# Kernel optimization log

Hardware: AMD Instinct MI355X
Metric: run time of the kernel (lower is better)

## Reference

```python
import jax, jax.numpy as jnp
import numpy as np

LAM = 0.5
LAG = 1
ALPHA = 0.5
EPS = 1e-8


def setup_inputs() -> dict:
    key = jax.random.key(0)
    k1, k2, k3, k4 = jax.random.split(key, 4)
    B, T, F, H = 64, 4096, 64, 256
    return {
        "input": jax.random.normal(k1, (B, T, 1), dtype=jnp.float32),
        "target": jax.random.normal(k2, (B, T, 1), dtype=jnp.float32),
        "sequence": jax.random.normal(k3, (B, T, F), dtype=jnp.float32),
        "forget_gates": jax.random.uniform(k4, (B, T, H), dtype=jnp.float32),
    }


def reference(input, target, sequence, forget_gates):
    B, T, F = sequence.shape
    x = jnp.moveaxis(sequence, 1, 0)          # [T, B, F] time-major
    x_t = x[LAG:]                              # [T-LAG, B, F]
    x_lag = x[:-LAG]                           # [T-LAG, B, F]

    m0 = jnp.zeros((B, F), dtype=sequence.dtype)
    v0 = jnp.full((B, F), EPS, dtype=sequence.dtype)
    c0 = jnp.zeros((B, F), dtype=sequence.dtype)

    def step(carry, inp):
        m, v, c = carry
        xt, xl = inp
        m = LAM * m + (1.0 - LAM) * xt
        v = LAM * v + (1.0 - LAM) * (xt - m) ** 2
        c = LAM * c + (1.0 - LAM) * (xt - m) * (xl - m)
        ac = c / jnp.sqrt(v * v + EPS)         # matches torch: sqrt(var*var + eps)
        return (m, v, c), ac

    _, acs = jax.lax.scan(step, (m0, v0, c0), (x_t, x_lag))  # [T-LAG, B, F]
    pad = jnp.zeros((LAG, B, F), dtype=sequence.dtype)       # initial_padding zeros
    ac_full = jnp.concatenate([pad, acs], axis=0)            # [T, B, F]

    irrelevance = 1.0 - jnp.abs(ac_full)                     # [T, B, F]
    irrelevance = jnp.mean(irrelevance, axis=2, keepdims=True)  # [T, B, 1]
    irrelevance = jnp.moveaxis(irrelevance, 0, 1)            # [B, T, 1]

    penalty = jnp.mean(irrelevance * forget_gates)
    mse = jnp.mean((input - target) ** 2)
    return mse + ALPHA * penalty
```

## Files before the change

### kernel.cpp

```cpp
#include <hip/hip_runtime.h>

constexpr int B = 64;
constexpr int T = 4096;
constexpr int F = 64;
constexpr int H = 256;
constexpr float EPSC = 1e-8f;
constexpr float ALPHAC = 0.5f;

constexpr int C = 128;
constexpr int W = 48;
constexpr int CHUNKS = T / C;
constexpr int NTASK = B * CHUNKS;
constexpr int SCAN_BLOCKS = NTASK / 4;
constexpr int TILE = 32;

constexpr int DOT_BLOCKS = 2048;

#define WS_IRR 0
#define WS_PEN (B * T)
#define WS_MSE (B * T + DOT_BLOCKS)

__global__ __launch_bounds__(256) void k_scan(
    const float* __restrict__ seq,
    const float* __restrict__ inp,
    const float* __restrict__ tgt,
    float* __restrict__ ws) {
  __shared__ float lt[4][TILE][65];
  const int lane = threadIdx.x & 63;
  const int wv = threadIdx.x >> 6;
  const int task = blockIdx.x * 4 + wv;
  const int b = task / CHUNKS;
  const int ci = task % CHUNKS;
  const int t0 = ci * C;

  const float* sp = seq + (size_t)b * T * F + lane;

  float m = 0.f, v = 0.f, c = 0.f;
  float xl = 0.f;

  if (ci == 0) {
    v = EPSC;
  } else {
    const int ts = t0 - W;
    xl = sp[(ts - 1) * F];
    float xw[4];
#pragma unroll
    for (int j = 0; j < 4; ++j) xw[j] = sp[(ts + j) * F];
#pragma unroll
    for (int i = 0; i < W; ++i) {
      const float xt = xw[i & 3];
      if (i + 4 < W) xw[i & 3] = sp[(ts + i + 4) * F];
      m = 0.5f * (m + xt);
      const float d = xt - m;
      v = 0.5f * fmaf(d, d, v);
      c = 0.5f * fmaf(d, xl - m, c);
      xl = xt;
    }
  }

  float xb[8];
#pragma unroll
  for (int j = 0; j < 8; ++j) xb[j] = sp[(t0 + j) * F];

  const int tr = lane & 31;
  const int half = lane >> 5;

  for (int tile = 0; tile < C / TILE; ++tile) {
    const int ibase = tile * TILE;
#pragma unroll
    for (int j = 0; j < TILE; ++j) {
      const int i = ibase + j;
      const int tt = t0 + i;
      const float xt = xb[j & 7];
      int tp = i + 8;
      tp = (tp < C) ? tp : (C - 1);
      xb[j & 7] = sp[(t0 + tp) * F];
      float w;
      if (tt != 0) {
        m = 0.5f * (m + xt);
        const float d = xt - m;
        v = 0.5f * fmaf(d, d, v);
        c = 0.5f * fmaf(d, xl - m, c);
        const float ac = c * rsqrtf(fmaf(v, v, EPSC));
        w = 1.0f - fabsf(ac);
      } else {
        w = 1.0f;
      }
      xl = xt;
      lt[wv][j][lane] = w;
    }
    __syncthreads();
    float s = 0.f;
#pragma unroll
    for (int k = 0; k < 32; ++k) s += lt[wv][tr][half * 32 + k];
    s += __shfl_xor(s, 32, 64);
    if (half == 0) ws[WS_IRR + b * T + t0 + ibase + tr] = s;
    __syncthreads();
  }

  float macc = 0.f;
  const int gid = blockIdx.x * blockDim.x + threadIdx.x;
  const int nt = gridDim.x * blockDim.x;
  const int R = B * T;
  for (int i = gid; i < R; i += nt) {
    const float d = inp[i] - tgt[i];
    macc = fmaf(d, d, macc);
  }
#pragma unroll
  for (int off = 32; off; off >>= 1) macc += __shfl_xor(macc, off, 64);
  __shared__ float sm[4];
  if (lane == 0) sm[wv] = macc;
  __syncthreads();
  if (threadIdx.x == 0)
    ws[WS_MSE + blockIdx.x] = (sm[0] + sm[1]) + (sm[2] + sm[3]);
}

__global__ __launch_bounds__(256) void k_dot(
    const float* __restrict__ fg,
    float* __restrict__ ws) {
  const float* __restrict__ irr = ws + WS_IRR;
  const float4* __restrict__ fg4 = reinterpret_cast<const float4*>(fg);
  constexpr int N4 = B * T * (H / 4);
  constexpr int STRIDE = DOT_BLOCKS * 256;
  const int gid = blockIdx.x * 256 + threadIdx.x;
  float acc = 0.f;
#pragma unroll 4
  for (int i = gid; i < N4; i += STRIDE) {
    const float4 q = fg4[i];
    const float r = irr[i >> 6];
    acc = fmaf((q.x + q.y) + (q.z + q.w), r, acc);
  }
#pragma unroll
  for (int off = 32; off; off >>= 1) acc += __shfl_xor(acc, off, 64);
  __shared__ float sm[4];
  if ((threadIdx.x & 63) == 0) sm[threadIdx.x >> 6] = acc;
  __syncthreads();
  if (threadIdx.x == 0)
    ws[WS_PEN + blockIdx.x] = (sm[0] + sm[1]) + (sm[2] + sm[3]);
}

__global__ __launch_bounds__(256) void k_reduce(
    const float* __restrict__ ws,
    float* __restrict__ out) {
  float p = 0.f, mt = 0.f;
#pragma unroll
  for (int i = 0; i < DOT_BLOCKS / 256; ++i)
    p += ws[WS_PEN + threadIdx.x + i * 256];
#pragma unroll
  for (int i = 0; i < SCAN_BLOCKS / 256; ++i)
    mt += ws[WS_MSE + threadIdx.x + i * 256];
#pragma unroll
  for (int off = 32; off; off >>= 1) {
    p += __shfl_xor(p, off, 64);
    mt += __shfl_xor(mt, off, 64);
  }
  __shared__ float sm[8];
  if ((threadIdx.x & 63) == 0) {
    sm[(threadIdx.x >> 6) * 2] = p;
    sm[(threadIdx.x >> 6) * 2 + 1] = mt;
  }
  __syncthreads();
  if (threadIdx.x == 0) {
    const float pt = sm[0] + sm[2] + sm[4] + sm[6];
    const float ms = sm[1] + sm[3] + sm[5] + sm[7];
    const float R = (float)B * (float)T;
    const float pscale = ALPHAC / (R * (float)H * (float)F);
    out[0] = ms / R + pt * pscale;
  }
}

extern "C" void kernel_launch(void* const* d_in, const int* in_sizes, int n_in,
                              void* d_out, int out_size, void* d_ws, size_t ws_size,
                              hipStream_t stream) {
  const float* inp = (const float*)d_in[0];
  const float* tgt = (const float*)d_in[1];
  const float* seq = (const float*)d_in[2];
  const float* fg  = (const float*)d_in[3];
  float* out = (float*)d_out;
  float* ws  = (float*)d_ws;

  k_scan<<<SCAN_BLOCKS, 256, 0, stream>>>(seq, inp, tgt, ws);
  k_dot<<<DOT_BLOCKS, 256, 0, stream>>>(fg, ws);
  k_reduce<<<1, 256, 0, stream>>>(ws, out);
}
```

Before: 412.1 us.

## Fuse forget-gate dot product into the scan kernel and drop irrelevance buffer

Removes the separate dot kernel. Each wave now streams its own batch/chunk slice of forget_gates, with a 4-deep float4 prefetch, while it runs the recurrence. It multiplies the per-timestep irrelevance sums by the gate row sums in registers. This avoids writing and re-reading the irrelevance array and saves one kernel launch, and it lets the large forget-gate read overlap with the latency-bound scan. In exchange the block-level barriers are dropped in favour of wave-local shared memory, and register pressure rises (32-element g array plus prefetch buffers). The full gate read now also depends on the relatively few scan waves, which may limit how much bandwidth it can reach.

```diff
diff --git a/kernel.cpp b/kernel.cpp
--- a/kernel.cpp
+++ b/kernel.cpp
@@ -11,21 +11,20 @@
 constexpr int W = 48;
 constexpr int CHUNKS = T / C;
 constexpr int NTASK = B * CHUNKS;
-constexpr int SCAN_BLOCKS = NTASK / 4;
+constexpr int K_BLOCKS = NTASK / 4;
 constexpr int TILE = 32;
 
-constexpr int DOT_BLOCKS = 2048;
+#define WS_PEN 0
+#define WS_MSE NTASK
 
-#define WS_IRR 0
-#define WS_PEN (B * T)
-#define WS_MSE (B * T + DOT_BLOCKS)
-
-__global__ __launch_bounds__(256) void k_scan(
+__global__ __launch_bounds__(256) void k_fused(
     const float* __restrict__ seq,
+    const float* __restrict__ fg,
     const float* __restrict__ inp,
     const float* __restrict__ tgt,
     float* __restrict__ ws) {
   __shared__ float lt[4][TILE][65];
+  __shared__ float ls[4][2][TILE];
   const int lane = threadIdx.x & 63;
   const int wv = threadIdx.x >> 6;
   const int task = blockIdx.x * 4 + wv;
@@ -34,6 +33,7 @@
   const int t0 = ci * C;
 
   const float* sp = seq + (size_t)b * T * F + lane;
+  const float* gp = fg + (size_t)b * T * H + lane * 4;
 
   float m = 0.f, v = 0.f, c = 0.f;
   float xl = 0.f;
@@ -58,12 +58,18 @@
     }
   }
 
+  float4 qb[4];
   float xb[8];
+#pragma unroll
+  for (int j = 0; j < 4; ++j)
+    qb[j] = *reinterpret_cast<const float4*>(gp + (size_t)(t0 + j) * H);
 #pragma unroll
   for (int j = 0; j < 8; ++j) xb[j] = sp[(t0 + j) * F];
 
   const int tr = lane & 31;
   const int half = lane >> 5;
+  float g[TILE];
+  float acc = 0.f, acc2 = 0.f;
 
   for (int tile = 0; tile < C / TILE; ++tile) {
     const int ibase = tile * TILE;
@@ -71,10 +77,17 @@
     for (int j = 0; j < TILE; ++j) {
       const int i = ibase + j;
       const int tt = t0 + i;
-      const float xt = xb[j & 7];
+      const float4 q = qb[i & 3];
+      const float xt = xb[i & 7];
+      int tq = i + 4;
+      tq = (tq < C) ? tq : (C - 1);
+      qb[i & 3] = *reinterpret_cast<const float4*>(gp + (size_t)(t0 + tq) * H);
       int tp = i + 8;
       tp = (tp < C) ? tp : (C - 1);
-      xb[j & 7] = sp[(t0 + tp) * F];
+      xb[i & 7] = sp[(t0 + tp) * F];
+
+      g[j] = (q.x + q.y) + (q.z + q.w);
+
       float w;
       if (tt != 0) {
         m = 0.5f * (m + xt);
@@ -89,14 +102,21 @@
       xl = xt;
       lt[wv][j][lane] = w;
     }
-    __syncthreads();
     float s = 0.f;
 #pragma unroll
     for (int k = 0; k < 32; ++k) s += lt[wv][tr][half * 32 + k];
-    s += __shfl_xor(s, 32, 64);
-    if (half == 0) ws[WS_IRR + b * T + t0 + ibase + tr] = s;
-    __syncthreads();
+    ls[wv][half][tr] = s;
+#pragma unroll
+    for (int j = 0; j < TILE; j += 2) {
+      acc  = fmaf(ls[wv][0][j]     + ls[wv][1][j],     g[j],     acc);
+      acc2 = fmaf(ls[wv][0][j + 1] + ls[wv][1][j + 1], g[j + 1], acc2);
+    }
   }
+  acc += acc2;
+
+#pragma unroll
+  for (int off = 32; off; off >>= 1) acc += __shfl_xor(acc, off, 64);
+  if (lane == 0) ws[WS_PEN + task] = acc;
 
   float macc = 0.f;
   const int gid = blockIdx.x * blockDim.x + threadIdx.x;
@@ -115,39 +135,15 @@
     ws[WS_MSE + blockIdx.x] = (sm[0] + sm[1]) + (sm[2] + sm[3]);
 }
 
-__global__ __launch_bounds__(256) void k_dot(
-    const float* __restrict__ fg,
-    float* __restrict__ ws) {
-  const float* __restrict__ irr = ws + WS_IRR;
-  const float4* __restrict__ fg4 = reinterpret_cast<const float4*>(fg);
-  constexpr int N4 = B * T * (H / 4);
-  constexpr int STRIDE = DOT_BLOCKS * 256;
-  const int gid = blockIdx.x * 256 + threadIdx.x;
-  float acc = 0.f;
-#pragma unroll 4
-  for (int i = gid; i < N4; i += STRIDE) {
-    const float4 q = fg4[i];
-    const float r = irr[i >> 6];
-    acc = fmaf((q.x + q.y) + (q.z + q.w), r, acc);
-  }
-#pragma unroll
-  for (int off = 32; off; off >>= 1) acc += __shfl_xor(acc, off, 64);
-  __shared__ float sm[4];
-  if ((threadIdx.x & 63) == 0) sm[threadIdx.x >> 6] = acc;
-  __syncthreads();
-  if (threadIdx.x == 0)
-    ws[WS_PEN + blockIdx.x] = (sm[0] + sm[1]) + (sm[2] + sm[3]);
-}
-
 __global__ __launch_bounds__(256) void k_reduce(
     const float* __restrict__ ws,
     float* __restrict__ out) {
   float p = 0.f, mt = 0.f;
 #pragma unroll
-  for (int i = 0; i < DOT_BLOCKS / 256; ++i)
+  for (int i = 0; i < NTASK / 256; ++i)
     p += ws[WS_PEN + threadIdx.x + i * 256];
 #pragma unroll
-  for (int i = 0; i < SCAN_BLOCKS / 256; ++i)
+  for (int i = 0; i < K_BLOCKS / 256; ++i)
     mt += ws[WS_MSE + threadIdx.x + i * 256];
 #pragma unroll
   for (int off = 32; off; off >>= 1) {
@@ -179,7 +175,6 @@
   float* out = (float*)d_out;
   float* ws  = (float*)d_ws;
 
-  k_scan<<<SCAN_BLOCKS, 256, 0, stream>>>(seq, inp, tgt, ws);
-  k_dot<<<DOT_BLOCKS, 256, 0, stream>>>(fg, ws);
+  k_fused<<<K_BLOCKS, 256, 0, stream>>>(seq, fg, inp, tgt, ws);
   k_reduce<<<1, 256, 0, stream>>>(ws, out);
 }
```

New measurement: 406.8 us. No clear change (-1.3%).
